# Optimization experiments

Hardware: AMD Instinct MI355X
Metric: run time of the kernel (lower is better)

Reference implementation:

```python
import jax, jax.numpy as jnp
import numpy as np

NUM_Q_HEADS = 16
NUM_KV_HEADS = 4
GROUP_SIZE = NUM_Q_HEADS // NUM_KV_HEADS  # 4
GROUP_DIM = 128                           # head dim, also RoPE dim
THETA = 10000.0


def _rope_cos_sin(num_tokens, dim, dtype):
    # freqs = 1/theta^(2i/d); angles[t, i] = t * freqs[i]
    inv_freq = 1.0 / (THETA ** (jnp.arange(0, dim, 2, dtype=jnp.float32) / dim))
    t = jnp.arange(num_tokens, dtype=jnp.float32)
    angles = jnp.outer(t, inv_freq)  # [N, d/2]
    # broadcast to [N, 1, 1, d/2] to match q/k shape [B, N, gs, kvh, d/2]
    cos = jnp.cos(angles)[:, None, None, :].astype(dtype)
    sin = jnp.sin(angles)[:, None, None, :].astype(dtype)
    return cos, sin


def _apply_rope(x, cos, sin):
    # x: [B, N, gs, kvh, d]; complex rotation on interleaved (even, odd) pairs
    xr = x.reshape(*x.shape[:-1], -1, 2)
    xe, xo = xr[..., 0], xr[..., 1]
    oe = xe * cos - xo * sin
    oo = xe * sin + xo * cos
    return jnp.stack([oe, oo], axis=-1).reshape(x.shape)


def setup_inputs() -> dict:
    key = jax.random.key(0)
    ks = jax.random.split(key, 5)
    B, N, D = 1, 2048, 2048
    KV_D = GROUP_DIM * NUM_KV_HEADS  # 512
    s = 0.02
    return {
        "x": jax.random.normal(ks[0], (B, N, D), dtype=jnp.float32),
        "Wq": jax.random.normal(ks[1], (D, D), dtype=jnp.float32) * s,
        "Wk": jax.random.normal(ks[2], (D, KV_D), dtype=jnp.float32) * s,
        "Wv": jax.random.normal(ks[3], (D, KV_D), dtype=jnp.float32) * s,
        "Wo": jax.random.normal(ks[4], (D, D), dtype=jnp.float32) * s,
    }


def reference(x, Wq, Wk, Wv, Wo):
    B, N, D = x.shape
    d = GROUP_DIM
    # projections
    q = (x @ Wq).reshape(B, N, GROUP_SIZE, NUM_KV_HEADS, d)
    k = (x @ Wk).reshape(B, N, 1, NUM_KV_HEADS, d)
    v = (x @ Wv).reshape(B, N, 1, NUM_KV_HEADS, d)
    # RoPE (interleaved complex rotation)
    cos, sin = _rope_cos_sin(N, d, x.dtype)
    q = _apply_rope(q, cos, sin)
    k = _apply_rope(k, cos, sin)
    # to [B, kvh, gs, N, d] / [B, kvh, N, d]
    q = jnp.transpose(q, (0, 3, 2, 1, 4))        # b k s n d
    k = jnp.transpose(k[:, :, 0], (0, 2, 1, 3))  # b k m d
    v = jnp.transpose(v[:, :, 0], (0, 2, 1, 3))  # b k m d
    scores = jnp.einsum('bksnd,bkmd->bksnm', q, k)
    causal = jnp.tril(jnp.ones((N, N), dtype=bool))
    scores = jnp.where(causal, scores, -jnp.inf)
    weights = jax.nn.softmax(scores / jnp.sqrt(jnp.asarray(d, x.dtype)), axis=-1)
    ctx = jnp.einsum('bksnm,bkmd->bksnd', weights, v)   # [B, kvh, gs, N, d]
    # flatten heads (kvh-major, matching torch flatten(1,2)), then [B, N, D]
    ctx = ctx.reshape(B, NUM_KV_HEADS * GROUP_SIZE, N, d)
    ctx = jnp.transpose(ctx, (0, 2, 1, 3)).reshape(B, N, D)
    return ctx @ Wo
```

## Files before the change

kernel.cpp:

```cpp
#include <hip/hip_runtime.h>

typedef unsigned short u16;
typedef float f32x4 __attribute__((ext_vector_type(4)));
typedef short s16x8 __attribute__((ext_vector_type(8)));
typedef short s16x4 __attribute__((ext_vector_type(4)));

__device__ __forceinline__ u16 f2b(float f) {
  union { float f; unsigned u; } v; v.f = f;
  unsigned r = v.u + 0x7fffu + ((v.u >> 16) & 1u);
  return (u16)(r >> 16);
}
__device__ __forceinline__ float b2f(u16 b) {
  union { unsigned u; float f; } v; v.u = ((unsigned)b) << 16;
  return v.f;
}
__device__ __forceinline__ f32x4 mfma_bf16(s16x8 a, s16x8 b, f32x4 c) {
  return __builtin_amdgcn_mfma_f32_16x16x32_bf16(a, b, c, 0, 0, 0);
}
__device__ __forceinline__ void gl_lds16(const u16* g, u16* l) {
  __builtin_amdgcn_global_load_lds(
      (const __attribute__((address_space(1))) void*)g,
      (__attribute__((address_space(3))) void*)l, 16, 0, 0);
}

__global__ void conv_x(const float* __restrict__ in, u16* __restrict__ out, int n) {
  int i = (blockIdx.x * 256 + threadIdx.x) * 8;
  if (i >= n) return;
  f32x4 a = *(const f32x4*)(in + i);
  f32x4 b = *(const f32x4*)(in + i + 4);
  s16x8 o = {(short)f2b(a.x), (short)f2b(a.y), (short)f2b(a.z), (short)f2b(a.w),
             (short)f2b(b.x), (short)f2b(b.y), (short)f2b(b.z), (short)f2b(b.w)};
  *(s16x8*)(out + i) = o;
}

__global__ void transW(const float* __restrict__ Wq, const float* __restrict__ Wk,
                       const float* __restrict__ Wv, const float* __restrict__ Wo,
                       u16* __restrict__ WqkvT, u16* __restrict__ WoT) {
  __shared__ u16 tile[64][68];
  const int z = blockIdx.z;
  if (z == 1 && blockIdx.x >= 32) return;
  const int ox = blockIdx.x * 64;
  const int oy = blockIdx.y * 64;
  const float* src; int scol, C; u16* dst;
  if (z == 0) {
    if (ox < 2048)      { src = Wq; scol = ox;        C = 2048; }
    else if (ox < 2560) { src = Wk; scol = ox - 2048; C = 512;  }
    else                { src = Wv; scol = ox - 2560; C = 512;  }
    dst = WqkvT;
  } else { src = Wo; scol = ox; C = 2048; dst = WoT; }
  const int t = threadIdx.x, lr = t >> 4, c4 = (t & 15) * 4;
#pragma unroll
  for (int p = 0; p < 4; ++p) {
    int r = p * 16 + lr;
    f32x4 v = *(const f32x4*)(src + (size_t)(oy + r) * C + scol + c4);
    s16x4 pk = {(short)f2b(v.x), (short)f2b(v.y), (short)f2b(v.z), (short)f2b(v.w)};
    *(s16x4*)(&tile[r][c4]) = pk;
  }
  __syncthreads();
#pragma unroll
  for (int q = 0; q < 4; ++q) {
    int oc = q * 16 + lr;
    s16x4 pk = {(short)tile[c4 + 0][oc], (short)tile[c4 + 1][oc],
                (short)tile[c4 + 2][oc], (short)tile[c4 + 3][oc]};
    *(s16x4*)(dst + (size_t)(ox + oc) * 2048 + oy + c4) = pk;
  }
}

__global__ void transpose_v(const u16* __restrict__ qkv, u16* __restrict__ vT) {
  __shared__ u16 tile[64][68];
  const int bx = blockIdx.x * 64;
  const int by = blockIdx.y * 64;
  const int t = threadIdx.x, lr = t >> 4, c4 = (t & 15) * 4;
#pragma unroll
  for (int p = 0; p < 4; ++p) {
    int r = p * 16 + lr;
    s16x4 v = *(const s16x4*)(qkv + (size_t)(by + r) * 3072 + 2560 + bx + c4);
    *(s16x4*)(&tile[r][c4]) = v;
  }
  __syncthreads();
#pragma unroll
  for (int q = 0; q < 4; ++q) {
    int oc = q * 16 + lr;
    s16x4 pk = {(short)tile[c4 + 0][oc], (short)tile[c4 + 1][oc],
                (short)tile[c4 + 2][oc], (short)tile[c4 + 3][oc]};
    *(s16x4*)(vT + (size_t)(bx + oc) * 2048 + by + c4) = pk;
  }
}

__device__ __forceinline__ void gemm_core(const u16* __restrict__ A,
                                          const u16* __restrict__ Bt,
                                          int K, int m0, int n0,
                                          f32x4 (*acc)[4], u16* As, u16* Bs) {
  const int t = threadIdx.x;
  const int wave = t >> 6, lane = t & 63, quad = lane >> 4, lc = lane & 15;
  const int wm = (wave >> 1) * 64, wn = (wave & 1) * 64;
  for (int k0 = 0; k0 < K; k0 += 32) {
#pragma unroll
    for (int h = 0; h < 2; ++h) {
      int ch = h * 256 + t, row = ch >> 2, kc = (ch & 3) * 8;
      gl_lds16(A  + (size_t)(m0 + row) * K + k0 + kc, As + (size_t)(h * 256 + wave * 64) * 8);
      gl_lds16(Bt + (size_t)(n0 + row) * K + k0 + kc, Bs + (size_t)(h * 256 + wave * 64) * 8);
    }
    __syncthreads();
    s16x8 af[4], bfr[4];
#pragma unroll
    for (int i = 0; i < 4; ++i)
      af[i] = *(const s16x8*)(As + (wm + i * 16 + lc) * 32 + quad * 8);
#pragma unroll
    for (int j = 0; j < 4; ++j)
      bfr[j] = *(const s16x8*)(Bs + (wn + j * 16 + lc) * 32 + quad * 8);
#pragma unroll
    for (int i = 0; i < 4; ++i)
#pragma unroll
      for (int j = 0; j < 4; ++j)
        acc[i][j] = mfma_bf16(af[i], bfr[j], acc[i][j]);
    __syncthreads();
  }
}

__global__ __launch_bounds__(256, 2) void gemm_qkv(const u16* __restrict__ A,
                                                   const u16* __restrict__ Bt,
                                                   u16* __restrict__ C) {
  __shared__ __align__(16) u16 As[128 * 32];
  __shared__ __align__(16) u16 Bs[128 * 32];
  const int n0 = blockIdx.x * 128, m0 = blockIdx.y * 128;
  const int lane = threadIdx.x & 63, wave = threadIdx.x >> 6;
  const int quad = lane >> 4, lc = lane & 15;
  const int wm = (wave >> 1) * 64, wn = (wave & 1) * 64;
  const f32x4 z = {0.f, 0.f, 0.f, 0.f};
  f32x4 acc[4][4];
#pragma unroll
  for (int i = 0; i < 4; ++i)
#pragma unroll
    for (int j = 0; j < 4; ++j) acc[i][j] = z;
  gemm_core(A, Bt, 2048, m0, n0, acc, As, Bs);
#pragma unroll
  for (int j = 0; j < 4; ++j) {
    const int colbase = wn + j * 16;
    const bool rope = (n0 + colbase) < 2560;
    const int col = n0 + colbase + lc;
    const int ip = ((colbase + lc) & 127) >> 1;
    const float inv_freq = exp2f(-0.20762050593046014f * (float)ip);
#pragma unroll
    for (int i = 0; i < 4; ++i)
#pragma unroll
      for (int r = 0; r < 4; ++r) {
        float v = acc[i][j][r];
        float p = __shfl_xor(v, 1);
        float val = v;
        if (rope) {
          int token = m0 + wm + i * 16 + quad * 4 + r;
          float ang = (float)token * inv_freq;
          float sv, cv;
          sincosf(ang, &sv, &cv);
          val = (lc & 1) ? (p * sv + v * cv) : (v * cv - p * sv);
        }
        C[(size_t)(m0 + wm + i * 16 + quad * 4 + r) * 3072 + col] = f2b(val);
      }
  }
}

__global__ __launch_bounds__(256, 2) void gemm_out(const u16* __restrict__ A,
                                                   const u16* __restrict__ Bt,
                                                   float* __restrict__ C) {
  __shared__ __align__(16) u16 As[128 * 32];
  __shared__ __align__(16) u16 Bs[128 * 32];
  const int n0 = blockIdx.x * 128, m0 = blockIdx.y * 128;
  const int lane = threadIdx.x & 63, wave = threadIdx.x >> 6;
  const int quad = lane >> 4, lc = lane & 15;
  const int wm = (wave >> 1) * 64, wn = (wave & 1) * 64;
  const f32x4 z = {0.f, 0.f, 0.f, 0.f};
  f32x4 acc[4][4];
#pragma unroll
  for (int i = 0; i < 4; ++i)
#pragma unroll
    for (int j = 0; j < 4; ++j) acc[i][j] = z;
  gemm_core(A, Bt, 2048, m0, n0, acc, As, Bs);
#pragma unroll
  for (int i = 0; i < 4; ++i)
#pragma unroll
    for (int j = 0; j < 4; ++j)
#pragma unroll
      for (int r = 0; r < 4; ++r)
        C[(size_t)(m0 + wm + i * 16 + quad * 4 + r) * 2048 + n0 + wn + j * 16 + lc] =
            acc[i][j][r];
}

__global__ __launch_bounds__(256, 2) void attn_k(const u16* __restrict__ qkv,
                                                 const u16* __restrict__ vT,
                                                 u16* __restrict__ Opart,
                                                 float* __restrict__ Lpart) {
  const int bid = blockIdx.x;
  const int hq = bid / 40, idx = bid % 40;
  int qt, c;
  if (idx < 4)       { qt = idx;                          c = 0; }
  else if (idx < 12) { int w = idx - 4;  qt = 4 + (w >> 1);  c = w & 1; }
  else if (idx < 24) { int w = idx - 12; qt = 8 + w / 3;     c = w % 3; }
  else               { int w = idx - 24; qt = 12 + (w >> 2); c = w & 3; }
  const int s0 = c * 8;
  const int s1 = min(c * 8 + 8, 2 * qt + 2);

  const int kvh = hq & 3;
  const int qc0 = hq << 7, kc0 = 2048 + (kvh << 7), vr0 = kvh << 7;

  __shared__ __align__(16) u16 Ks[64 * 136];
  __shared__ __align__(16) u16 Vs[128 * 72];
  __shared__ __align__(16) u16 Ps[128 * 72];

  const int t = threadIdx.x, wave = t >> 6, lane = t & 63;
  const int quad = lane >> 4, lc = lane & 15;
  const int kr = t >> 4, kc = (t & 15) * 8;
  const int vr = t >> 3, vc = (t & 7) * 8;

  s16x8 qf[2][4];
#pragma unroll
  for (int i = 0; i < 2; ++i)
#pragma unroll
    for (int ks = 0; ks < 4; ++ks)
      qf[i][ks] = *(const s16x8*)(qkv +
          (size_t)(qt * 128 + wave * 32 + i * 16 + lc) * 3072 +
          qc0 + ks * 32 + quad * 8);

  const f32x4 z = {0.f, 0.f, 0.f, 0.f};
  f32x4 oa[2][8];
#pragma unroll
  for (int i = 0; i < 2; ++i)
#pragma unroll
    for (int n = 0; n < 8; ++n) oa[i][n] = z;
  float Ls[2][4] = {{0.f, 0.f, 0.f, 0.f}, {0.f, 0.f, 0.f, 0.f}};
  const float scale2 = 0.12751744545f;

  s16x8 kpf[4], vpf[4];
  {
    const int j0 = s0 * 64;
#pragma unroll
    for (int p = 0; p < 4; ++p)
      kpf[p] = *(const s16x8*)(qkv + (size_t)(j0 + p * 16 + kr) * 3072 + kc0 + kc);
#pragma unroll
    for (int p = 0; p < 4; ++p)
      vpf[p] = *(const s16x8*)(vT + (size_t)(vr0 + p * 32 + vr) * 2048 + j0 + vc);
  }

  for (int tile = s0; tile < s1; ++tile) {
    const int j0 = tile * 64;
    __syncthreads();
#pragma unroll
    for (int p = 0; p < 4; ++p)
      *(s16x8*)(Ks + (p * 16 + kr) * 136 + kc) = kpf[p];
#pragma unroll
    for (int p = 0; p < 4; ++p)
      *(s16x8*)(Vs + (p * 32 + vr) * 72 + vc) = vpf[p];
    __syncthreads();
    if (tile + 1 < s1) {
      const int j1 = j0 + 64;
#pragma unroll
      for (int p = 0; p < 4; ++p)
        kpf[p] = *(const s16x8*)(qkv + (size_t)(j1 + p * 16 + kr) * 3072 + kc0 + kc);
#pragma unroll
      for (int p = 0; p < 4; ++p)
        vpf[p] = *(const s16x8*)(vT + (size_t)(vr0 + p * 32 + vr) * 2048 + j1 + vc);
    }
    f32x4 sa[2][4];
#pragma unroll
    for (int i = 0; i < 2; ++i)
#pragma unroll
      for (int n = 0; n < 4; ++n) sa[i][n] = z;
#pragma unroll
    for (int ks = 0; ks < 4; ++ks)
#pragma unroll
      for (int n = 0; n < 4; ++n) {
        s16x8 bf = *(const s16x8*)(Ks + (n * 16 + lc) * 136 + ks * 32 + quad * 8);
        sa[0][n] = mfma_bf16(qf[0][ks], bf, sa[0][n]);
        sa[1][n] = mfma_bf16(qf[1][ks], bf, sa[1][n]);
      }
#pragma unroll
    for (int i = 0; i < 2; ++i) {
      const int qrow_base = qt * 128 + wave * 32 + i * 16 + quad * 4;
#pragma unroll
      for (int n = 0; n < 4; ++n) {
        int jc = j0 + n * 16 + lc;
#pragma unroll
        for (int r = 0; r < 4; ++r) {
          float e = (jc <= qrow_base + r) ? exp2f(sa[i][n][r] * scale2) : 0.f;
          Ps[(wave * 32 + i * 16 + quad * 4 + r) * 72 + n * 16 + lc] = f2b(e);
          Ls[i][r] += e;
        }
      }
    }
#pragma unroll
    for (int ks = 0; ks < 2; ++ks)
#pragma unroll
      for (int i = 0; i < 2; ++i) {
        s16x8 af = *(const s16x8*)(Ps + (wave * 32 + i * 16 + lc) * 72 +
                                   ks * 32 + quad * 8);
#pragma unroll
        for (int n = 0; n < 8; ++n) {
          s16x8 bf = *(const s16x8*)(Vs + (n * 16 + lc) * 72 + ks * 32 + quad * 8);
          oa[i][n] = mfma_bf16(af, bf, oa[i][n]);
        }
      }
  }
#pragma unroll
  for (int i = 0; i < 2; ++i)
#pragma unroll
    for (int r = 0; r < 4; ++r) {
      float s = Ls[i][r];
      s += __shfl_xor(s, 1);
      s += __shfl_xor(s, 2);
      s += __shfl_xor(s, 4);
      s += __shfl_xor(s, 8);
      Ls[i][r] = s;
    }
  u16* Ob = Opart + (size_t)bid * (128 * 128);
  if (lc == 0) {
#pragma unroll
    for (int i = 0; i < 2; ++i)
#pragma unroll
      for (int r = 0; r < 4; ++r)
        Lpart[(size_t)bid * 128 + wave * 32 + i * 16 + quad * 4 + r] = Ls[i][r];
  }
#pragma unroll
  for (int i = 0; i < 2; ++i)
#pragma unroll
    for (int n = 0; n < 8; ++n)
#pragma unroll
      for (int r = 0; r < 4; ++r)
        Ob[(wave * 32 + i * 16 + quad * 4 + r) * 128 + n * 16 + lc] =
            f2b(oa[i][n][r]);
}

__global__ void attn_combine(const u16* __restrict__ Opart,
                             const float* __restrict__ Lpart,
                             u16* __restrict__ ctx) {
  const int hq = blockIdx.y, kvh = hq & 3, sg = hq >> 2;
  const int lin = blockIdx.x * 256 + threadIdx.x;
  const int token = lin >> 4, d8 = (lin & 15) << 3;
  const int qt = token >> 7, row = token & 127;
  const int tier = qt >> 2;
  const int btab[4] = {0, 4, 12, 24};
  const int base = hq * 40 + btab[tier] + (qt & 3) * (tier + 1);
  const int cnt = tier + 1;
  float acc[8] = {0.f, 0.f, 0.f, 0.f, 0.f, 0.f, 0.f, 0.f};
  float L = 0.f;
  for (int c = 0; c < cnt; ++c) {
    const int b = base + c;
    L += Lpart[(size_t)b * 128 + row];
    s16x8 o = *(const s16x8*)(Opart + (size_t)b * 16384 + row * 128 + d8);
#pragma unroll
    for (int i = 0; i < 8; ++i) acc[i] += b2f((u16)o[i]);
  }
  const float inv = 1.f / L;
  s16x8 out;
#pragma unroll
  for (int i = 0; i < 8; ++i) out[i] = (short)f2b(acc[i] * inv);
  *(s16x8*)(ctx + (size_t)token * 2048 + ((kvh * 4 + sg) << 7) + d8) = out;
}

extern "C" void kernel_launch(void* const* d_in, const int* in_sizes, int n_in,
                              void* d_out, int out_size, void* d_ws, size_t ws_size,
                              hipStream_t stream) {
  const float* x  = (const float*)d_in[0];
  const float* Wq = (const float*)d_in[1];
  const float* Wk = (const float*)d_in[2];
  const float* Wv = (const float*)d_in[3];
  const float* Wo = (const float*)d_in[4];

  char* w = (char*)d_ws;
  u16* qkvb   = (u16*)w;  w += (size_t)2048 * 3072 * 2;
  u16* vTb    = (u16*)w;  w += (size_t)512 * 2048 * 2;
  u16* WoT    = (u16*)w;  w += (size_t)2048 * 2048 * 2;
  u16* ctxb   = (u16*)w;  w += (size_t)2048 * 2048 * 2;
  float* Lpart= (float*)w; w += (size_t)640 * 128 * 4;
  u16* Opart  = (u16*)w;
  u16* xb     = (u16*)w;  w += (size_t)2048 * 2048 * 2;
  u16* WqkvT  = (u16*)w;  w += (size_t)3072 * 2048 * 2;
  w += (size_t)2 * 1024 * 1024;

  conv_x<<<2048, 256, 0, stream>>>(x, xb, 2048 * 2048);
  transW<<<dim3(48, 32, 2), 256, 0, stream>>>(Wq, Wk, Wv, Wo, WqkvT, WoT);

  gemm_qkv<<<dim3(24, 16), 256, 0, stream>>>(xb, WqkvT, qkvb);

  transpose_v<<<dim3(8, 32), 256, 0, stream>>>(qkvb, vTb);

  attn_k<<<640, 256, 0, stream>>>(qkvb, vTb, Opart, Lpart);
  attn_combine<<<dim3(128, 16), 256, 0, stream>>>(Opart, Lpart, ctxb);

  gemm_out<<<dim3(16, 16), 256, 0, stream>>>(ctxb, WoT, (float*)d_out);
}
```

Baseline: 253.2 us.

## Split-K both projection GEMMs with separate reduce kernels and RoPE epilogue

Both the QKV and output GEMMs are split along K into two halves, doubling the grid so more CUs are busy (384→768 and 256→512 blocks). The halves write bf16 partials, and new reduce kernels sum them, with RoPE moved into the QKV reduce. The Wo transpose now runs just before the output GEMM, and the workspace is reorganized to alias buffers. This adds extra launches and partial-buffer traffic, and rounds partials to bf16, which loses precision, especially on the fp32 output.

Measured after the change: 239.3 us. 5.5% less time.

```diff
diff --git a/kernel.cpp b/kernel.cpp
--- a/kernel.cpp
+++ b/kernel.cpp
@@ -33,21 +33,15 @@
   *(s16x8*)(out + i) = o;
 }
 
-__global__ void transW(const float* __restrict__ Wq, const float* __restrict__ Wk,
-                       const float* __restrict__ Wv, const float* __restrict__ Wo,
-                       u16* __restrict__ WqkvT, u16* __restrict__ WoT) {
+__global__ void transW_qkv(const float* __restrict__ Wq, const float* __restrict__ Wk,
+                           const float* __restrict__ Wv, u16* __restrict__ WqkvT) {
   __shared__ u16 tile[64][68];
-  const int z = blockIdx.z;
-  if (z == 1 && blockIdx.x >= 32) return;
   const int ox = blockIdx.x * 64;
   const int oy = blockIdx.y * 64;
-  const float* src; int scol, C; u16* dst;
-  if (z == 0) {
-    if (ox < 2048)      { src = Wq; scol = ox;        C = 2048; }
-    else if (ox < 2560) { src = Wk; scol = ox - 2048; C = 512;  }
-    else                { src = Wv; scol = ox - 2560; C = 512;  }
-    dst = WqkvT;
-  } else { src = Wo; scol = ox; C = 2048; dst = WoT; }
+  const float* src; int scol, C;
+  if (ox < 2048)      { src = Wq; scol = ox;        C = 2048; }
+  else if (ox < 2560) { src = Wk; scol = ox - 2048; C = 512;  }
+  else                { src = Wv; scol = ox - 2560; C = 512;  }
   const int t = threadIdx.x, lr = t >> 4, c4 = (t & 15) * 4;
 #pragma unroll
   for (int p = 0; p < 4; ++p) {
@@ -62,14 +56,34 @@
     int oc = q * 16 + lr;
     s16x4 pk = {(short)tile[c4 + 0][oc], (short)tile[c4 + 1][oc],
                 (short)tile[c4 + 2][oc], (short)tile[c4 + 3][oc]};
-    *(s16x4*)(dst + (size_t)(ox + oc) * 2048 + oy + c4) = pk;
+    *(s16x4*)(WqkvT + (size_t)(ox + oc) * 2048 + oy + c4) = pk;
+  }
+}
+
+__global__ void transW_o(const float* __restrict__ Wo, u16* __restrict__ WoT) {
+  __shared__ u16 tile[64][68];
+  const int ox = blockIdx.x * 64, oy = blockIdx.y * 64;
+  const int t = threadIdx.x, lr = t >> 4, c4 = (t & 15) * 4;
+#pragma unroll
+  for (int p = 0; p < 4; ++p) {
+    int r = p * 16 + lr;
+    f32x4 v = *(const f32x4*)(Wo + (size_t)(oy + r) * 2048 + ox + c4);
+    s16x4 pk = {(short)f2b(v.x), (short)f2b(v.y), (short)f2b(v.z), (short)f2b(v.w)};
+    *(s16x4*)(&tile[r][c4]) = pk;
+  }
+  __syncthreads();
+#pragma unroll
+  for (int q = 0; q < 4; ++q) {
+    int oc = q * 16 + lr;
+    s16x4 pk = {(short)tile[c4 + 0][oc], (short)tile[c4 + 1][oc],
+                (short)tile[c4 + 2][oc], (short)tile[c4 + 3][oc]};
+    *(s16x4*)(WoT + (size_t)(ox + oc) * 2048 + oy + c4) = pk;
   }
 }
 
 __global__ void transpose_v(const u16* __restrict__ qkv, u16* __restrict__ vT) {
   __shared__ u16 tile[64][68];
-  const int bx = blockIdx.x * 64;
-  const int by = blockIdx.y * 64;
+  const int bx = blockIdx.x * 64, by = blockIdx.y * 64;
   const int t = threadIdx.x, lr = t >> 4, c4 = (t & 15) * 4;
 #pragma unroll
   for (int p = 0; p < 4; ++p) {
@@ -89,12 +103,13 @@
 
 __device__ __forceinline__ void gemm_core(const u16* __restrict__ A,
                                           const u16* __restrict__ Bt,
-                                          int K, int m0, int n0,
+                                          int kbeg, int kend, int K,
+                                          int m0, int n0,
                                           f32x4 (*acc)[4], u16* As, u16* Bs) {
   const int t = threadIdx.x;
   const int wave = t >> 6, lane = t & 63, quad = lane >> 4, lc = lane & 15;
   const int wm = (wave >> 1) * 64, wn = (wave & 1) * 64;
-  for (int k0 = 0; k0 < K; k0 += 32) {
+  for (int k0 = kbeg; k0 < kend; k0 += 32) {
 #pragma unroll
     for (int h = 0; h < 2; ++h) {
       int ch = h * 256 + t, row = ch >> 2, kc = (ch & 3) * 8;
@@ -118,11 +133,12 @@
   }
 }
 
-__global__ __launch_bounds__(256, 2) void gemm_qkv(const u16* __restrict__ A,
-                                                   const u16* __restrict__ Bt,
-                                                   u16* __restrict__ C) {
+__global__ __launch_bounds__(256, 2) void gemm_qkv_half(const u16* __restrict__ A,
+                                                        const u16* __restrict__ Bt,
+                                                        u16* __restrict__ P) {
   __shared__ __align__(16) u16 As[128 * 32];
   __shared__ __align__(16) u16 Bs[128 * 32];
+  const int kh = blockIdx.z;
   const int n0 = blockIdx.x * 128, m0 = blockIdx.y * 128;
   const int lane = threadIdx.x & 63, wave = threadIdx.x >> 6;
   const int quad = lane >> 4, lc = lane & 15;
@@ -133,38 +149,52 @@
   for (int i = 0; i < 4; ++i)
 #pragma unroll
     for (int j = 0; j < 4; ++j) acc[i][j] = z;
-  gemm_core(A, Bt, 2048, m0, n0, acc, As, Bs);
-#pragma unroll
-  for (int j = 0; j < 4; ++j) {
-    const int colbase = wn + j * 16;
-    const bool rope = (n0 + colbase) < 2560;
-    const int col = n0 + colbase + lc;
-    const int ip = ((colbase + lc) & 127) >> 1;
-    const float inv_freq = exp2f(-0.20762050593046014f * (float)ip);
-#pragma unroll
-    for (int i = 0; i < 4; ++i)
-#pragma unroll
-      for (int r = 0; r < 4; ++r) {
-        float v = acc[i][j][r];
-        float p = __shfl_xor(v, 1);
-        float val = v;
-        if (rope) {
-          int token = m0 + wm + i * 16 + quad * 4 + r;
-          float ang = (float)token * inv_freq;
-          float sv, cv;
-          sincosf(ang, &sv, &cv);
-          val = (lc & 1) ? (p * sv + v * cv) : (v * cv - p * sv);
-        }
-        C[(size_t)(m0 + wm + i * 16 + quad * 4 + r) * 3072 + col] = f2b(val);
-      }
-  }
-}
-
-__global__ __launch_bounds__(256, 2) void gemm_out(const u16* __restrict__ A,
-                                                   const u16* __restrict__ Bt,
-                                                   float* __restrict__ C) {
+  gemm_core(A, Bt, kh * 1024, kh * 1024 + 1024, 2048, m0, n0, acc, As, Bs);
+  u16* Pk = P + (size_t)kh * (2048 * 3072);
+#pragma unroll
+  for (int i = 0; i < 4; ++i)
+#pragma unroll
+    for (int j = 0; j < 4; ++j)
+#pragma unroll
+      for (int r = 0; r < 4; ++r)
+        Pk[(size_t)(m0 + wm + i * 16 + quad * 4 + r) * 3072 + n0 + wn + j * 16 + lc] =
+            f2b(acc[i][j][r]);
+}
+
+__global__ void reduce_rope(const u16* __restrict__ P, u16* __restrict__ qkv) {
+  const int lin = blockIdx.x * 256 + threadIdx.x;
+  const int row = lin / 384, c8 = (lin - row * 384) * 8;
+  const u16* p0 = P + (size_t)row * 3072 + c8;
+  s16x8 a = *(const s16x8*)p0;
+  s16x8 b = *(const s16x8*)(p0 + 6291456);
+  float v[8];
+#pragma unroll
+  for (int i = 0; i < 8; ++i) v[i] = b2f((u16)a[i]) + b2f((u16)b[i]);
+  if (c8 < 2560) {
+#pragma unroll
+    for (int h = 0; h < 4; ++h) {
+      const int i = 2 * h;
+      const int ip = ((c8 + i) & 127) >> 1;
+      const float ang = (float)row * exp2f(-0.20762050593046014f * (float)ip);
+      float sv, cv;
+      sincosf(ang, &sv, &cv);
+      const float e = v[i], o = v[i + 1];
+      v[i]     = e * cv - o * sv;
+      v[i + 1] = e * sv + o * cv;
+    }
+  }
+  s16x8 o;
+#pragma unroll
+  for (int i = 0; i < 8; ++i) o[i] = (short)f2b(v[i]);
+  *(s16x8*)(qkv + (size_t)row * 3072 + c8) = o;
+}
+
+__global__ __launch_bounds__(256, 2) void gemm_out_half(const u16* __restrict__ A,
+                                                        const u16* __restrict__ Bt,
+                                                        u16* __restrict__ Po) {
   __shared__ __align__(16) u16 As[128 * 32];
   __shared__ __align__(16) u16 Bs[128 * 32];
+  const int kh = blockIdx.z;
   const int n0 = blockIdx.x * 128, m0 = blockIdx.y * 128;
   const int lane = threadIdx.x & 63, wave = threadIdx.x >> 6;
   const int quad = lane >> 4, lc = lane & 15;
@@ -175,15 +205,30 @@
   for (int i = 0; i < 4; ++i)
 #pragma unroll
     for (int j = 0; j < 4; ++j) acc[i][j] = z;
-  gemm_core(A, Bt, 2048, m0, n0, acc, As, Bs);
+  gemm_core(A, Bt, kh * 1024, kh * 1024 + 1024, 2048, m0, n0, acc, As, Bs);
+  u16* Pk = Po + (size_t)kh * (2048 * 2048);
 #pragma unroll
   for (int i = 0; i < 4; ++i)
 #pragma unroll
     for (int j = 0; j < 4; ++j)
 #pragma unroll
       for (int r = 0; r < 4; ++r)
-        C[(size_t)(m0 + wm + i * 16 + quad * 4 + r) * 2048 + n0 + wn + j * 16 + lc] =
-            acc[i][j][r];
+        Pk[(size_t)(m0 + wm + i * 16 + quad * 4 + r) * 2048 + n0 + wn + j * 16 + lc] =
+            f2b(acc[i][j][r]);
+}
+
+__global__ void reduce_out(const u16* __restrict__ Po, float* __restrict__ out) {
+  const int lin = blockIdx.x * 256 + threadIdx.x;
+  const u16* p0 = Po + (size_t)lin * 8;
+  s16x8 a = *(const s16x8*)p0;
+  s16x8 b = *(const s16x8*)(p0 + 4194304);
+  f32x4 o0, o1;
+#pragma unroll
+  for (int i = 0; i < 4; ++i) o0[i] = b2f((u16)a[i]) + b2f((u16)b[i]);
+#pragma unroll
+  for (int i = 0; i < 4; ++i) o1[i] = b2f((u16)a[i + 4]) + b2f((u16)b[i + 4]);
+  *(f32x4*)(out + (size_t)lin * 8) = o0;
+  *(f32x4*)(out + (size_t)lin * 8 + 4) = o1;
 }
 
 __global__ __launch_bounds__(256, 2) void attn_k(const u16* __restrict__ qkv,
@@ -365,26 +410,30 @@
   const float* Wv = (const float*)d_in[3];
   const float* Wo = (const float*)d_in[4];
 
-  char* w = (char*)d_ws;
-  u16* qkvb   = (u16*)w;  w += (size_t)2048 * 3072 * 2;
-  u16* vTb    = (u16*)w;  w += (size_t)512 * 2048 * 2;
-  u16* WoT    = (u16*)w;  w += (size_t)2048 * 2048 * 2;
-  u16* ctxb   = (u16*)w;  w += (size_t)2048 * 2048 * 2;
-  float* Lpart= (float*)w; w += (size_t)640 * 128 * 4;
-  u16* Opart  = (u16*)w;
-  u16* xb     = (u16*)w;  w += (size_t)2048 * 2048 * 2;
-  u16* WqkvT  = (u16*)w;  w += (size_t)3072 * 2048 * 2;
-  w += (size_t)2 * 1024 * 1024;
+  char* base = (char*)d_ws;
+  u16*   xb    = (u16*)(base);
+  u16*   qkvb  = (u16*)(base);
+  u16*   WoT   = (u16*)(base);
+  u16*   WqkvT = (u16*)(base + 8388608);
+  u16*   vTb   = (u16*)(base + 12582912);
+  float* Lpart = (float*)(base + 14680064);
+  u16*   Pq    = (u16*)(base + 20971520);
+  u16*   Opart = (u16*)(base + 20971520);
+  u16*   Po    = (u16*)(base + 20971520);
+  u16*   ctxb  = (u16*)(base + 41943040);
 
   conv_x<<<2048, 256, 0, stream>>>(x, xb, 2048 * 2048);
-  transW<<<dim3(48, 32, 2), 256, 0, stream>>>(Wq, Wk, Wv, Wo, WqkvT, WoT);
-
-  gemm_qkv<<<dim3(24, 16), 256, 0, stream>>>(xb, WqkvT, qkvb);
+  transW_qkv<<<dim3(48, 32), 256, 0, stream>>>(Wq, Wk, Wv, WqkvT);
+
+  gemm_qkv_half<<<dim3(24, 16, 2), 256, 0, stream>>>(xb, WqkvT, Pq);
+  reduce_rope<<<3072, 256, 0, stream>>>(Pq, qkvb);
 
   transpose_v<<<dim3(8, 32), 256, 0, stream>>>(qkvb, vTb);
 
   attn_k<<<640, 256, 0, stream>>>(qkvb, vTb, Opart, Lpart);
   attn_combine<<<dim3(128, 16), 256, 0, stream>>>(Opart, Lpart, ctxb);
 
-  gemm_out<<<dim3(16, 16), 256, 0, stream>>>(ctxb, WoT, (float*)d_out);
-}
+  transW_o<<<dim3(32, 32), 256, 0, stream>>>(Wo, WoT);
+  gemm_out_half<<<dim3(16, 16, 2), 256, 0, stream>>>(ctxb, WoT, Po);
+  reduce_out<<<2048, 256, 0, stream>>>(Po, (float*)d_out);
+}
```
